# Kernel tuning notes

Hardware: AMD Instinct MI355X
Metric: run time of the kernel (lower is better)

The kernel has to match this reference:

```python
import jax, jax.numpy as jnp
import numpy as np

B, N, DIM = 4, 2048, 128
HEADS, HEAD = 8, 128
INNER = HEADS * HEAD  # 1024
EPS = 1e-5


def setup_inputs() -> dict:
    key = jax.random.key(0)
    k0, k1, k2 = jax.random.split(key, 3)
    return {
        "x": jax.random.normal(k0, (B, N, DIM), jnp.float32),
        "ln_gamma": jnp.ones((DIM,), jnp.float32),
        "ln_beta": jnp.zeros((DIM,), jnp.float32),
        "w_qkv": jax.random.normal(k1, (3 * INNER, DIM), jnp.float32) * (DIM ** -0.5),
        "w_out": jax.random.normal(k2, (DIM, INNER), jnp.float32) * (INNER ** -0.5),
        "b_out": jnp.zeros((DIM,), jnp.float32),
    }


def _rope(t):
    """lucidrains-style rotary embedding over full last dim of t: [b,h,n,d]."""
    n, d = t.shape[-2], t.shape[-1]
    inv_freq = 1.0 / (10000.0 ** (jnp.arange(0, d, 2, dtype=jnp.float32) / d))
    freqs = jnp.arange(n, dtype=jnp.float32)[:, None] * inv_freq[None, :]  # [n, d/2]
    freqs = jnp.repeat(freqs, 2, axis=-1)  # interleaved duplicate -> [n, d]
    cos, sin = jnp.cos(freqs), jnp.sin(freqs)
    # rotate_half on interleaved pairs: (x1, x2) -> (-x2, x1)
    x1, x2 = t[..., 0::2], t[..., 1::2]
    rot = jnp.stack((-x2, x1), axis=-1).reshape(t.shape)
    return t * cos + rot * sin


def reference(x, ln_gamma, ln_beta, w_qkv, w_out, b_out):
    # LayerNorm
    mu = x.mean(-1, keepdims=True)
    var = x.var(-1, keepdims=True)
    xn = (x - mu) * jax.lax.rsqrt(var + EPS) * ln_gamma + ln_beta
    # QKV projection (bias-free)
    qkv = jnp.einsum('bnd,ed->bne', xn, w_qkv)  # [B, N, 3*INNER]
    q, k, v = jnp.split(qkv, 3, axis=-1)
    to_heads = lambda t: t.reshape(B, N, HEADS, HEAD).transpose(0, 2, 1, 3)
    q, k, v = to_heads(q), to_heads(k), to_heads(v)  # [B, H, N, HEAD]
    # Partial RoPE: rotate all but the last token; last token stays unrotated
    q = jnp.concatenate([_rope(q[:, :, :-1]), q[:, :, -1:]], axis=2)
    k = jnp.concatenate([_rope(k[:, :, :-1]), k[:, :, -1:]], axis=2)
    scale = HEAD ** -0.5
    dots = jnp.einsum('bhid,bhjd->bhij', q, k) * scale  # [B, H, N, N]
    attn = jax.nn.softmax(dots, axis=-1)
    out = jnp.einsum('bhij,bhjd->bhid', attn, v)
    out = out.transpose(0, 2, 1, 3).reshape(B, N, INNER)
    return out @ w_out.T + b_out
```

## Files before the change

kernel.cpp:

```cpp
#include <hip/hip_runtime.h>
#include <hip/hip_bf16.h>
#include <hip/hip_fp16.h>

#define B_      4
#define N_      2048
#define DIM_    128
#define HEADS_  8
#define HEAD_   128
#define INNER_  1024
#define QKV_    3072
#define EPS_    1e-5f
#define SCALE_  0.08838834764831845f
#define ROPE_C  0.20762050593046015f

typedef __attribute__((ext_vector_type(8))) short short8;
typedef __attribute__((ext_vector_type(4))) short short4v;
typedef __attribute__((ext_vector_type(4))) float f32x4;


__device__ __forceinline__ unsigned short f2bf(float f) {
    unsigned u = __builtin_bit_cast(unsigned, f);
    u = (u + 0x7fffu + ((u >> 16) & 1u)) >> 16;
    return (unsigned short)u;
}
__device__ __forceinline__ float bf2f(unsigned short h) {
    unsigned u = ((unsigned)h) << 16;
    return __builtin_bit_cast(float, u);
}
__device__ __forceinline__ unsigned pk2(float a, float b) {
    return (unsigned)f2bf(a) | ((unsigned)f2bf(b) << 16);
}
__device__ __forceinline__ short4v pack4(const float* e) {
    __hip_bfloat162 h0 = __float22bfloat162_rn(make_float2(e[0], e[1]));
    __hip_bfloat162 h1 = __float22bfloat162_rn(make_float2(e[2], e[3]));
    uint2 u;
    __builtin_memcpy(&u.x, &h0, 4);
    __builtin_memcpy(&u.y, &h1, 4);
    return __builtin_bit_cast(short4v, u);
}

__global__ __launch_bounds__(256) void k_prep(
    const float* __restrict__ x, const float* __restrict__ g,
    const float* __restrict__ be, const float* __restrict__ w_qkv,
    const float* __restrict__ w_out, unsigned short* __restrict__ xnb,
    unsigned short* __restrict__ wqb, unsigned short* __restrict__ wob)
{
    const int bid = blockIdx.x;
    if (bid < 2048) {
        const int w = threadIdx.x >> 6, l = threadIdx.x & 63;
        const int row = bid * 4 + w;
        float2 v = *(const float2*)(x + (size_t)row * 128 + l * 2);
        float s = v.x + v.y, s2 = v.x * v.x + v.y * v.y;
#pragma unroll
        for (int off = 1; off < 64; off <<= 1) {
            s  += __shfl_xor(s, off);
            s2 += __shfl_xor(s2, off);
        }
        float mu = s * (1.f / 128.f);
        float var = s2 * (1.f / 128.f) - mu * mu;
        float rs = rsqrtf(var + EPS_);
        float2 gg = *(const float2*)(g + l * 2);
        float2 bb = *(const float2*)(be + l * 2);
        float ox = (v.x - mu) * rs * gg.x + bb.x;
        float oy = (v.y - mu) * rs * gg.y + bb.y;
        *(unsigned*)(xnb + (size_t)row * 128 + l * 2) = pk2(ox, oy);
    } else if (bid < 2240) {
        size_t i = ((size_t)(bid - 2048) * 256 + threadIdx.x) * 8;
        float4 f0 = *(const float4*)(w_qkv + i), f1 = *(const float4*)(w_qkv + i + 4);
        uint4 u = { pk2(f0.x, f0.y), pk2(f0.z, f0.w), pk2(f1.x, f1.y), pk2(f1.z, f1.w) };
        *(uint4*)(wqb + i) = u;
    } else {
        size_t i = ((size_t)(bid - 2240) * 256 + threadIdx.x) * 8;
        float4 f0 = *(const float4*)(w_out + i), f1 = *(const float4*)(w_out + i + 4);
        uint4 u = { pk2(f0.x, f0.y), pk2(f0.z, f0.w), pk2(f1.x, f1.y), pk2(f1.z, f1.w) };
        *(uint4*)(wob + i) = u;
    }
}

__global__ __launch_bounds__(256) void k_qkvf(
    const unsigned short* __restrict__ xnb, const unsigned short* __restrict__ wb,
    unsigned short* __restrict__ Q, unsigned short* __restrict__ K,
    unsigned short* __restrict__ Vt)
{
    __shared__ unsigned short lA[128 * 128];
    __shared__ unsigned short lB[128 * 128];
    const int t = threadIdx.x;
    const int wv = t >> 6, l = t & 63;
    const int lm = l & 15, quad = l >> 4;
    const int row0 = blockIdx.x * 128;
    const int by   = blockIdx.y;
    const int e0   = by * 128;

#pragma unroll
    for (int i = 0; i < 8; ++i) {
        int c = t + 256 * i;  int r = c >> 4, c8 = c & 15;
        int sc = (c8 ^ (r & 7)) * 8;
        *(uint4*)&lA[r * 128 + sc] =
            *(const uint4*)(xnb + (size_t)(row0 + r) * 128 + c8 * 8);
        *(uint4*)&lB[r * 128 + sc] =
            *(const uint4*)(wb + (size_t)(e0 + r) * 128 + c8 * 8);
    }
    __syncthreads();

    short8 af[2][4];
#pragma unroll
    for (int mt = 0; mt < 2; ++mt)
#pragma unroll
        for (int ks = 0; ks < 4; ++ks) {
            int r = wv * 32 + mt * 16 + lm;
            af[mt][ks] = *(short8*)&lA[r * 128 + (((ks * 4 + quad) ^ (r & 7)) << 3)];
        }

    f32x4 acc[2][8];
#pragma unroll
    for (int mt = 0; mt < 2; ++mt)
#pragma unroll
        for (int ct = 0; ct < 8; ++ct) acc[mt][ct] = (f32x4){0.f, 0.f, 0.f, 0.f};
#pragma unroll
    for (int ks = 0; ks < 4; ++ks) {
#pragma unroll
        for (int ct = 0; ct < 8; ++ct) {
            int r = ct * 16 + lm;
            short8 b = *(short8*)&lB[r * 128 + (((ks * 4 + quad) ^ (r & 7)) << 3)];
            acc[0][ct] = __builtin_amdgcn_mfma_f32_16x16x32_bf16(af[0][ks], b, acc[0][ct], 0, 0, 0);
            acc[1][ct] = __builtin_amdgcn_mfma_f32_16x16x32_bf16(af[1][ks], b, acc[1][ct], 0, 0, 0);
        }
    }
    __syncthreads();

    const int b  = row0 >> 11;
    const int n0 = row0 & (N_ - 1);
    const int h  = by & 7;
    const int bh = b * 8 + h;

    if (by < 16) {
#pragma unroll
        for (int mt = 0; mt < 2; ++mt)
#pragma unroll
            for (int ct = 0; ct < 8; ++ct)
#pragma unroll
                for (int r = 0; r < 4; ++r) {
                    int row = wv * 32 + mt * 16 + quad * 4 + r;
                    int chunk = ct * 2 + (lm >> 3);
                    lA[row * 128 + ((chunk ^ (row & 7)) << 3) + (lm & 7)] =
                        f2bf(acc[mt][ct][r]);
                }
        __syncthreads();

        const int r_loc = t >> 1, half = t & 1;
        const int n = n0 + r_loc;
        unsigned short* dst = (by < 8 ? Q : K) +
            ((size_t)bh * N_ + n) * HEAD_ + half * 64;
        const bool dorope = (n != N_ - 1);
#pragma unroll
        for (int j = 0; j < 8; ++j) {
            short8 vv = *(short8*)&lA[r_loc * 128 + (((half * 8 + j) ^ (r_loc & 7)) << 3)];
            if (dorope) {
                unsigned short* pv = (unsigned short*)&vv;
#pragma unroll
                for (int p = 0; p < 4; ++p) {
                    int i0 = half * 32 + j * 4 + p;
                    float invf = exp2f(-(float)i0 * ROPE_C);
                    float th = (float)n * invf;
                    float cs = __cosf(th), sn = __sinf(th);
                    float e = bf2f(pv[2 * p]), o = bf2f(pv[2 * p + 1]);
                    pv[2 * p]     = f2bf(e * cs - o * sn);
                    pv[2 * p + 1] = f2bf(o * cs + e * sn);
                }
            }
            *(short8*)(dst + j * 8) = vv;
        }
    } else {
#pragma unroll
        for (int mt = 0; mt < 2; ++mt)
#pragma unroll
            for (int ct = 0; ct < 8; ++ct)
#pragma unroll
                for (int r = 0; r < 4; ++r) {
                    int row = ct * 16 + lm;
                    int chunk = wv * 4 + quad;
                    lA[row * 128 + ((chunk ^ (row & 7)) << 3) + mt * 4 + r] =
                        f2bf(acc[mt][ct][r]);
                }
        __syncthreads();

        const int d = t >> 1, half = t & 1;
        unsigned short* dst = Vt + ((size_t)bh * HEAD_ + d) * N_ + n0 + half * 64;
#pragma unroll
        for (int j = 0; j < 8; ++j)
            *(short8*)(dst + j * 8) =
                *(short8*)&lA[d * 128 + (((half * 8 + j) ^ (d & 7)) << 3)];
    }
}

__global__ __launch_bounds__(256) void k_attn(
    const unsigned short* __restrict__ Q, const unsigned short* __restrict__ K,
    const unsigned short* __restrict__ Vt, unsigned short* __restrict__ Ob)
{
    __shared__ unsigned short lK[64 * 136];
    __shared__ unsigned short lV[128 * 68];

    const int t = threadIdx.x;
    const int w = t >> 6, l = t & 63;
    const int lm = l & 15, quad = l >> 4;
    const int bid = blockIdx.x;
    const int bh = bid & 31;
    const int qt = bid >> 5;
    const int n0 = qt * 128;
    const unsigned short* Qb = Q  + (size_t)bh * N_ * HEAD_;
    const unsigned short* Kb = K  + (size_t)bh * N_ * HEAD_;
    const unsigned short* Vb = Vt + (size_t)bh * N_ * HEAD_;

    short8 aq[2][4];
#pragma unroll
    for (int tt = 0; tt < 2; ++tt) {
        const unsigned short* qp =
            Qb + ((size_t)(n0 + tt * 64 + w * 16 + lm)) * 128 + quad * 8;
#pragma unroll
        for (int ks = 0; ks < 4; ++ks)
            aq[tt][ks] = *(const short8*)(qp + ks * 32);
    }

    f32x4 Oa[2][8];
#pragma unroll
    for (int tt = 0; tt < 2; ++tt)
#pragma unroll
        for (int i = 0; i < 8; ++i) Oa[tt][i] = (f32x4){0.f, 0.f, 0.f, 0.f};
    float ps0 = 0.f, ps1 = 0.f;
    const float C1 = SCALE_ * 1.44269504f;
    const float C0 = -23.08312f;

    short8 kr[4], vr[4];
#pragma unroll
    for (int i = 0; i < 4; ++i) {
        int c = t + 256 * i;
        kr[i] = *(const short8*)(Kb + ((size_t)(c >> 4)) * 128 + (c & 15) * 8);
        vr[i] = *(const short8*)(Vb + (size_t)(c >> 3) * N_ + (c & 7) * 8);
    }

    for (int jt = 0; jt < 32; ++jt) {
        __syncthreads();
#pragma unroll
        for (int i = 0; i < 4; ++i) {
            int c = t + 256 * i;
            *(short8*)&lK[(c >> 4) * 136 + (c & 15) * 8] = kr[i];
            *(short8*)&lV[(c >> 3) * 68  + (c & 7)  * 8] = vr[i];
        }
        __syncthreads();
        if (jt < 31) {
#pragma unroll
            for (int i = 0; i < 4; ++i) {
                int c = t + 256 * i;
                kr[i] = *(const short8*)(Kb + ((size_t)((jt + 1) * 64 + (c >> 4))) * 128 + (c & 15) * 8);
                vr[i] = *(const short8*)(Vb + (size_t)(c >> 3) * N_ + (jt + 1) * 64 + (c & 7) * 8);
            }
        }

        short4v pf0[4], pf1[4];
#pragma unroll
        for (int nb = 0; nb < 4; ++nb) {
            f32x4 st0 = (f32x4){0.f, 0.f, 0.f, 0.f};
            f32x4 st1 = (f32x4){0.f, 0.f, 0.f, 0.f};
#pragma unroll
            for (int ks = 0; ks < 4; ++ks) {
                short8 kf = *(short8*)&lK[(nb * 16 + lm) * 136 + ks * 32 + quad * 8];
                st0 = __builtin_amdgcn_mfma_f32_16x16x32_bf16(kf, aq[0][ks], st0, 0, 0, 0);
                st1 = __builtin_amdgcn_mfma_f32_16x16x32_bf16(kf, aq[1][ks], st1, 0, 0, 0);
            }
            float e0[4], e1[4];
#pragma unroll
            for (int r = 0; r < 4; ++r) {
                e0[r] = exp2f(st0[r] * C1 + C0);
                e1[r] = exp2f(st1[r] * C1 + C0);
                ps0 += e0[r];  ps1 += e1[r];
            }
            pf0[nb] = pack4(e0);
            pf1[nb] = pack4(e1);
        }

#pragma unroll
        for (int c2 = 0; c2 < 2; ++c2) {
            short8 ap0 = __builtin_shufflevector(pf0[2 * c2], pf0[2 * c2 + 1],
                                                 0, 1, 2, 3, 4, 5, 6, 7);
            short8 ap1 = __builtin_shufflevector(pf1[2 * c2], pf1[2 * c2 + 1],
                                                 0, 1, 2, 3, 4, 5, 6, 7);
#pragma unroll
            for (int nb8 = 0; nb8 < 8; ++nb8) {
                short8 bv = *(short8*)&lV[(nb8 * 16 + lm) * 68 + c2 * 32 + quad * 8];
                Oa[0][nb8] = __builtin_amdgcn_mfma_f32_16x16x32_bf16(ap0, bv, Oa[0][nb8], 0, 0, 0);
                Oa[1][nb8] = __builtin_amdgcn_mfma_f32_16x16x32_bf16(ap1, bv, Oa[1][nb8], 0, 0, 0);
            }
        }
    }

    ps0 += __shfl_xor(ps0, 16);  ps0 += __shfl_xor(ps0, 32);
    ps1 += __shfl_xor(ps1, 16);  ps1 += __shfl_xor(ps1, 32);

    const int b = bh >> 3, h = bh & 7;
#pragma unroll
    for (int tt = 0; tt < 2; ++tt)
#pragma unroll
        for (int r = 0; r < 4; ++r) {
            float lsum = __shfl(tt == 0 ? ps0 : ps1, (l & 48) | (quad * 4 + r));
            float il = 1.f / lsum;
            int n = n0 + tt * 64 + w * 16 + quad * 4 + r;
            unsigned short* op = Ob + ((size_t)b * N_ + n) * INNER_ + h * HEAD_ + lm;
#pragma unroll
            for (int nb8 = 0; nb8 < 8; ++nb8)
                op[nb8 * 16] = f2bf(Oa[tt][nb8][r] * il);
        }
}

__global__ __launch_bounds__(256) void k_proj(
    const unsigned short* __restrict__ Ob, const unsigned short* __restrict__ wob,
    const float* __restrict__ bias, float* __restrict__ out)
{
    __shared__ unsigned short lA[32 * 136];
    __shared__ unsigned short lB[64 * 136];
    float* lCf = (float*)lA;
    const int t = threadIdx.x;
    const int wv = t >> 6, l = t & 63;
    const int lm = l & 15, quad = l >> 4;
    const int rt = wv & 1, ch = wv >> 1;
    const int row0 = blockIdx.x * 32;
    const int e0   = blockIdx.y * 64;

    f32x4 acc[2];
#pragma unroll
    for (int ct = 0; ct < 2; ++ct) acc[ct] = (f32x4){0.f, 0.f, 0.f, 0.f};

    for (int kt = 0; kt < 8; ++kt) {
        __syncthreads();
#pragma unroll
        for (int i = 0; i < 2; ++i) {
            int c = t + 256 * i;  int r = c >> 4, c8 = c & 15;
            *(uint4*)&lA[r * 136 + c8 * 8] =
                *(const uint4*)(Ob + (size_t)(row0 + r) * 1024 + kt * 128 + c8 * 8);
        }
#pragma unroll
        for (int i = 0; i < 4; ++i) {
            int c = t + 256 * i;  int r = c >> 4, c8 = c & 15;
            *(uint4*)&lB[r * 136 + c8 * 8] =
                *(const uint4*)(wob + (size_t)(e0 + r) * 1024 + kt * 128 + c8 * 8);
        }
        __syncthreads();
        short8 a_[4];
#pragma unroll
        for (int ks = 0; ks < 4; ++ks)
            a_[ks] = *(short8*)&lA[(rt * 16 + lm) * 136 + ks * 32 + quad * 8];
#pragma unroll
        for (int ks = 0; ks < 4; ++ks)
#pragma unroll
            for (int ct = 0; ct < 2; ++ct) {
                short8 b = *(short8*)&lB[(ch * 32 + ct * 16 + lm) * 136 + ks * 32 + quad * 8];
                acc[ct] = __builtin_amdgcn_mfma_f32_16x16x32_bf16(a_[ks], b, acc[ct], 0, 0, 0);
            }
    }
    __syncthreads();
#pragma unroll
    for (int ct = 0; ct < 2; ++ct)
#pragma unroll
        for (int r = 0; r < 4; ++r)
            lCf[(rt * 16 + quad * 4 + r) * 68 + ch * 32 + ct * 16 + lm] = acc[ct][r];
    __syncthreads();
#pragma unroll
    for (int i = 0; i < 2; ++i) {
        int c = t + 256 * i;  int r = c >> 4, c4 = c & 15;
        float4 v = *(float4*)&lCf[r * 68 + c4 * 4];
        float4 b4 = *(const float4*)(bias + e0 + c4 * 4);
        v.x += b4.x; v.y += b4.y; v.z += b4.z; v.w += b4.w;
        *(float4*)(out + (size_t)(row0 + r) * 128 + e0 + c4 * 4) = v;
    }
}

extern "C" void kernel_launch(void* const* d_in, const int* in_sizes, int n_in,
                              void* d_out, int out_size, void* d_ws, size_t ws_size,
                              hipStream_t stream) {
    const float* x      = (const float*)d_in[0];
    const float* gamma  = (const float*)d_in[1];
    const float* beta   = (const float*)d_in[2];
    const float* w_qkv  = (const float*)d_in[3];
    const float* w_out  = (const float*)d_in[4];
    const float* b_out  = (const float*)d_in[5];
    float* out = (float*)d_out;
    char* wsb = (char*)d_ws;
    unsigned short* Q    = (unsigned short*)(wsb);
    unsigned short* K    = (unsigned short*)(wsb + (16ull << 20));
    unsigned short* Vt   = (unsigned short*)(wsb + (32ull << 20));
    unsigned short* Ob   = (unsigned short*)(wsb + (48ull << 20));
    unsigned short* xnb  = (unsigned short*)(wsb + (96ull << 20));
    unsigned short* wqb  = (unsigned short*)(wsb + (98ull << 20));
    unsigned short* wob  = (unsigned short*)(wsb + (99ull << 20));

    k_prep <<<dim3(2304),    256, 0, stream>>>(x, gamma, beta, w_qkv, w_out,
                                               xnb, wqb, wob);
    k_qkvf <<<dim3(64, 24),  256, 0, stream>>>(xnb, wqb, Q, K, Vt);
    k_attn <<<dim3(512),     256, 0, stream>>>(Q, K, Vt, Ob);
    k_proj <<<dim3(256, 2),  256, 0, stream>>>(Ob, wob, b_out, out);
}
```

Measured before the change: 188.7 us.

## Fuse LayerNorm and weight bf16 conversion into QKV and projection GEMM loads

Removes the separate prep kernel and instead computes LayerNorm on fp32 x while staging the A tile in the QKV GEMM, and converts fp32 weights to bf16 on the fly in both GEMMs. This saves one launch and the round trip of the bf16 intermediates through global memory. In exchange, each of the 24 column blocks redundantly recomputes LayerNorm for its rows, and the weight tiles are read as fp32, doubling the bytes loaded per tile. The epilogue staging moves from lA to lB so the A fragments are not overwritten.

```diff
diff --git a/kernel.cpp b/kernel.cpp
--- a/kernel.cpp
+++ b/kernel.cpp
@@ -39,46 +39,9 @@
     return __builtin_bit_cast(short4v, u);
 }
 
-__global__ __launch_bounds__(256) void k_prep(
+__global__ __launch_bounds__(256) void k_qkvf(
     const float* __restrict__ x, const float* __restrict__ g,
-    const float* __restrict__ be, const float* __restrict__ w_qkv,
-    const float* __restrict__ w_out, unsigned short* __restrict__ xnb,
-    unsigned short* __restrict__ wqb, unsigned short* __restrict__ wob)
-{
-    const int bid = blockIdx.x;
-    if (bid < 2048) {
-        const int w = threadIdx.x >> 6, l = threadIdx.x & 63;
-        const int row = bid * 4 + w;
-        float2 v = *(const float2*)(x + (size_t)row * 128 + l * 2);
-        float s = v.x + v.y, s2 = v.x * v.x + v.y * v.y;
-#pragma unroll
-        for (int off = 1; off < 64; off <<= 1) {
-            s  += __shfl_xor(s, off);
-            s2 += __shfl_xor(s2, off);
-        }
-        float mu = s * (1.f / 128.f);
-        float var = s2 * (1.f / 128.f) - mu * mu;
-        float rs = rsqrtf(var + EPS_);
-        float2 gg = *(const float2*)(g + l * 2);
-        float2 bb = *(const float2*)(be + l * 2);
-        float ox = (v.x - mu) * rs * gg.x + bb.x;
-        float oy = (v.y - mu) * rs * gg.y + bb.y;
-        *(unsigned*)(xnb + (size_t)row * 128 + l * 2) = pk2(ox, oy);
-    } else if (bid < 2240) {
-        size_t i = ((size_t)(bid - 2048) * 256 + threadIdx.x) * 8;
-        float4 f0 = *(const float4*)(w_qkv + i), f1 = *(const float4*)(w_qkv + i + 4);
-        uint4 u = { pk2(f0.x, f0.y), pk2(f0.z, f0.w), pk2(f1.x, f1.y), pk2(f1.z, f1.w) };
-        *(uint4*)(wqb + i) = u;
-    } else {
-        size_t i = ((size_t)(bid - 2240) * 256 + threadIdx.x) * 8;
-        float4 f0 = *(const float4*)(w_out + i), f1 = *(const float4*)(w_out + i + 4);
-        uint4 u = { pk2(f0.x, f0.y), pk2(f0.z, f0.w), pk2(f1.x, f1.y), pk2(f1.z, f1.w) };
-        *(uint4*)(wob + i) = u;
-    }
-}
-
-__global__ __launch_bounds__(256) void k_qkvf(
-    const unsigned short* __restrict__ xnb, const unsigned short* __restrict__ wb,
+    const float* __restrict__ be, const float* __restrict__ wq,
     unsigned short* __restrict__ Q, unsigned short* __restrict__ K,
     unsigned short* __restrict__ Vt)
 {
@@ -91,14 +54,63 @@
     const int by   = blockIdx.y;
     const int e0   = by * 128;
 
-#pragma unroll
-    for (int i = 0; i < 8; ++i) {
-        int c = t + 256 * i;  int r = c >> 4, c8 = c & 15;
-        int sc = (c8 ^ (r & 7)) * 8;
-        *(uint4*)&lA[r * 128 + sc] =
-            *(const uint4*)(xnb + (size_t)(row0 + r) * 128 + c8 * 8);
-        *(uint4*)&lB[r * 128 + sc] =
-            *(const uint4*)(wb + (size_t)(e0 + r) * 128 + c8 * 8);
+    {
+        const int r = t >> 1, half = t & 1;
+        const float* xr = x + (size_t)(row0 + r) * 128 + half * 64;
+        float sa[32], sq[32];
+#pragma unroll
+        for (int i = 0; i < 16; ++i) {
+            float4 v = *(const float4*)(xr + i * 4);
+            sa[2 * i]     = v.x + v.y;
+            sa[2 * i + 1] = v.z + v.w;
+            sq[2 * i]     = v.x * v.x + v.y * v.y;
+            sq[2 * i + 1] = v.z * v.z + v.w * v.w;
+        }
+#pragma unroll
+        for (int nlev = 16; nlev >= 1; nlev >>= 1)
+#pragma unroll
+            for (int j = 0; j < nlev; ++j) {
+                sa[j] = sa[2 * j] + sa[2 * j + 1];
+                sq[j] = sq[2 * j] + sq[2 * j + 1];
+            }
+        float s  = sa[0] + __shfl_xor(sa[0], 1);
+        float s2 = sq[0] + __shfl_xor(sq[0], 1);
+        float mu  = s * (1.f / 128.f);
+        float var = s2 * (1.f / 128.f) - mu * mu;
+        float rs  = rsqrtf(var + EPS_);
+#pragma unroll
+        for (int j = 0; j < 8; ++j) {
+            float4 a0 = *(const float4*)(xr + j * 8);
+            float4 a1 = *(const float4*)(xr + j * 8 + 4);
+            float4 g0 = *(const float4*)(g  + half * 64 + j * 8);
+            float4 g1 = *(const float4*)(g  + half * 64 + j * 8 + 4);
+            float4 b0 = *(const float4*)(be + half * 64 + j * 8);
+            float4 b1 = *(const float4*)(be + half * 64 + j * 8 + 4);
+            float e0_ = (a0.x - mu) * rs * g0.x + b0.x;
+            float e1_ = (a0.y - mu) * rs * g0.y + b0.y;
+            float e2_ = (a0.z - mu) * rs * g0.z + b0.z;
+            float e3_ = (a0.w - mu) * rs * g0.w + b0.w;
+            float e4_ = (a1.x - mu) * rs * g1.x + b1.x;
+            float e5_ = (a1.y - mu) * rs * g1.y + b1.y;
+            float e6_ = (a1.z - mu) * rs * g1.z + b1.z;
+            float e7_ = (a1.w - mu) * rs * g1.w + b1.w;
+            uint4 u = { pk2(e0_, e1_), pk2(e2_, e3_), pk2(e4_, e5_), pk2(e6_, e7_) };
+            int chunk = half * 8 + j;
+            *(uint4*)&lA[r * 128 + ((chunk ^ (r & 7)) << 3)] = u;
+        }
+    }
+    {
+        const int r = t >> 1, half = t & 1;
+        const float* wr = wq + (size_t)(e0 + r) * 128 + half * 64;
+#pragma unroll
+        for (int j = 0; j < 8; ++j) {
+            float4 a0 = *(const float4*)(wr + j * 8);
+            float4 a1 = *(const float4*)(wr + j * 8 + 4);
+            uint4 u = { pk2(a0.x, a0.y), pk2(a0.z, a0.w),
+                        pk2(a1.x, a1.y), pk2(a1.z, a1.w) };
+            int chunk = half * 8 + j;
+            *(uint4*)&lB[r * 128 + ((chunk ^ (r & 7)) << 3)] = u;
+        }
     }
     __syncthreads();
 
@@ -142,7 +154,7 @@
                 for (int r = 0; r < 4; ++r) {
                     int row = wv * 32 + mt * 16 + quad * 4 + r;
                     int chunk = ct * 2 + (lm >> 3);
-                    lA[row * 128 + ((chunk ^ (row & 7)) << 3) + (lm & 7)] =
+                    lB[row * 128 + ((chunk ^ (row & 7)) << 3) + (lm & 7)] =
                         f2bf(acc[mt][ct][r]);
                 }
         __syncthreads();
@@ -154,7 +166,7 @@
         const bool dorope = (n != N_ - 1);
 #pragma unroll
         for (int j = 0; j < 8; ++j) {
-            short8 vv = *(short8*)&lA[r_loc * 128 + (((half * 8 + j) ^ (r_loc & 7)) << 3)];
+            short8 vv = *(short8*)&lB[r_loc * 128 + (((half * 8 + j) ^ (r_loc & 7)) << 3)];
             if (dorope) {
                 unsigned short* pv = (unsigned short*)&vv;
 #pragma unroll
@@ -179,7 +191,7 @@
                 for (int r = 0; r < 4; ++r) {
                     int row = ct * 16 + lm;
                     int chunk = wv * 4 + quad;
-                    lA[row * 128 + ((chunk ^ (row & 7)) << 3) + mt * 4 + r] =
+                    lB[row * 128 + ((chunk ^ (row & 7)) << 3) + mt * 4 + r] =
                         f2bf(acc[mt][ct][r]);
                 }
         __syncthreads();
@@ -189,7 +201,7 @@
 #pragma unroll
         for (int j = 0; j < 8; ++j)
             *(short8*)(dst + j * 8) =
-                *(short8*)&lA[d * 128 + (((half * 8 + j) ^ (d & 7)) << 3)];
+                *(short8*)&lB[d * 128 + (((half * 8 + j) ^ (d & 7)) << 3)];
     }
 }
 
@@ -312,7 +324,7 @@
 }
 
 __global__ __launch_bounds__(256) void k_proj(
-    const unsigned short* __restrict__ Ob, const unsigned short* __restrict__ wob,
+    const unsigned short* __restrict__ Ob, const float* __restrict__ w_out,
     const float* __restrict__ bias, float* __restrict__ out)
 {
     __shared__ unsigned short lA[32 * 136];
@@ -337,11 +349,17 @@
             *(uint4*)&lA[r * 136 + c8 * 8] =
                 *(const uint4*)(Ob + (size_t)(row0 + r) * 1024 + kt * 128 + c8 * 8);
         }
-#pragma unroll
-        for (int i = 0; i < 4; ++i) {
-            int c = t + 256 * i;  int r = c >> 4, c8 = c & 15;
-            *(uint4*)&lB[r * 136 + c8 * 8] =
-                *(const uint4*)(wob + (size_t)(e0 + r) * 1024 + kt * 128 + c8 * 8);
+        {
+            const int r = t >> 2, q4 = t & 3;
+            const float* wr = w_out + (size_t)(e0 + r) * 1024 + kt * 128 + q4 * 32;
+#pragma unroll
+            for (int jj = 0; jj < 4; ++jj) {
+                float4 a0 = *(const float4*)(wr + jj * 8);
+                float4 a1 = *(const float4*)(wr + jj * 8 + 4);
+                uint4 u = { pk2(a0.x, a0.y), pk2(a0.z, a0.w),
+                            pk2(a1.x, a1.y), pk2(a1.z, a1.w) };
+                *(uint4*)&lB[r * 136 + q4 * 32 + jj * 8] = u;
+            }
         }
         __syncthreads();
         short8 a_[4];
@@ -388,13 +406,8 @@
     unsigned short* K    = (unsigned short*)(wsb + (16ull << 20));
     unsigned short* Vt   = (unsigned short*)(wsb + (32ull << 20));
     unsigned short* Ob   = (unsigned short*)(wsb + (48ull << 20));
-    unsigned short* xnb  = (unsigned short*)(wsb + (96ull << 20));
-    unsigned short* wqb  = (unsigned short*)(wsb + (98ull << 20));
-    unsigned short* wob  = (unsigned short*)(wsb + (99ull << 20));
-
-    k_prep <<<dim3(2304),    256, 0, stream>>>(x, gamma, beta, w_qkv, w_out,
-                                               xnb, wqb, wob);
-    k_qkvf <<<dim3(64, 24),  256, 0, stream>>>(xnb, wqb, Q, K, Vt);
-    k_attn <<<dim3(512),     256, 0, stream>>>(Q, K, Vt, Ob);
-    k_proj <<<dim3(256, 2),  256, 0, stream>>>(Ob, wob, b_out, out);
-}
+
+    k_qkvf <<<dim3(64, 24), 256, 0, stream>>>(x, gamma, beta, w_qkv, Q, K, Vt);
+    k_attn <<<dim3(512),    256, 0, stream>>>(Q, K, Vt, Ob);
+    k_proj <<<dim3(256, 2), 256, 0, stream>>>(Ob, w_out, b_out, out);
+}
```

Result: slower. 259.4 us (+37.5%).

## Switch attention kernel to 32x32x16 MFMA tiles with reshaped P/V fragments

Applied to the files above, without the earlier changes.

Rewrites the attention inner loop to use 32x32x16 bf16 MFMA instructions instead of 16x16x32. Each wave now owns 32 query rows, and scores, probabilities and output accumulators are laid out as 16-wide fragments. The V tile LDS stride moves from 68 to 72, and the V-transpose store in the QKV kernel is changed to match the new fragment layout. The goal is fewer MFMA issues and LDS fragment reads per unit of work, at the cost of different register pressure, a different LDS bank pattern, and scattered 2-byte output stores.

```diff
diff --git a/kernel.cpp b/kernel.cpp
--- a/kernel.cpp
+++ b/kernel.cpp
@@ -16,6 +16,7 @@
 typedef __attribute__((ext_vector_type(8))) short short8;
 typedef __attribute__((ext_vector_type(4))) short short4v;
 typedef __attribute__((ext_vector_type(4))) float f32x4;
+typedef __attribute__((ext_vector_type(16))) float f32x16;
 
 
 __device__ __forceinline__ unsigned short f2bf(float f) {
@@ -178,8 +179,9 @@
 #pragma unroll
                 for (int r = 0; r < 4; ++r) {
                     int row = ct * 16 + lm;
-                    int chunk = wv * 4 + quad;
-                    lA[row * 128 + ((chunk ^ (row & 7)) << 3) + mt * 4 + r] =
+                    int chunk = wv * 4 + mt * 2 + (quad & 1);
+                    int off   = (quad >> 1) * 4 + r;
+                    lA[row * 128 + ((chunk ^ (row & 7)) << 3) + off] =
                         f2bf(acc[mt][ct][r]);
                 }
         __syncthreads();
@@ -198,11 +200,11 @@
     const unsigned short* __restrict__ Vt, unsigned short* __restrict__ Ob)
 {
     __shared__ unsigned short lK[64 * 136];
-    __shared__ unsigned short lV[128 * 68];
+    __shared__ unsigned short lV[128 * 72];
 
     const int t = threadIdx.x;
     const int w = t >> 6, l = t & 63;
-    const int lm = l & 15, quad = l >> 4;
+    const int q32 = l & 31, hi = l >> 5;
     const int bid = blockIdx.x;
     const int bh = bid & 31;
     const int qt = bid >> 5;
@@ -211,22 +213,21 @@
     const unsigned short* Kb = K  + (size_t)bh * N_ * HEAD_;
     const unsigned short* Vb = Vt + (size_t)bh * N_ * HEAD_;
 
-    short8 aq[2][4];
-#pragma unroll
-    for (int tt = 0; tt < 2; ++tt) {
+    short8 aq[8];
+    {
         const unsigned short* qp =
-            Qb + ((size_t)(n0 + tt * 64 + w * 16 + lm)) * 128 + quad * 8;
-#pragma unroll
-        for (int ks = 0; ks < 4; ++ks)
-            aq[tt][ks] = *(const short8*)(qp + ks * 32);
-    }
-
-    f32x4 Oa[2][8];
-#pragma unroll
-    for (int tt = 0; tt < 2; ++tt)
-#pragma unroll
-        for (int i = 0; i < 8; ++i) Oa[tt][i] = (f32x4){0.f, 0.f, 0.f, 0.f};
-    float ps0 = 0.f, ps1 = 0.f;
+            Qb + (size_t)(n0 + w * 32 + q32) * 128 + hi * 8;
+#pragma unroll
+        for (int kc = 0; kc < 8; ++kc)
+            aq[kc] = *(const short8*)(qp + kc * 16);
+    }
+
+    f32x16 Oa[4];
+#pragma unroll
+    for (int i = 0; i < 4; ++i)
+        Oa[i] = (f32x16){0.f,0.f,0.f,0.f,0.f,0.f,0.f,0.f,
+                         0.f,0.f,0.f,0.f,0.f,0.f,0.f,0.f};
+    float ps = 0.f;
     const float C1 = SCALE_ * 1.44269504f;
     const float C0 = -23.08312f;
 
@@ -244,7 +245,7 @@
         for (int i = 0; i < 4; ++i) {
             int c = t + 256 * i;
             *(short8*)&lK[(c >> 4) * 136 + (c & 15) * 8] = kr[i];
-            *(short8*)&lV[(c >> 3) * 68  + (c & 7)  * 8] = vr[i];
+            *(short8*)&lV[(c >> 3) * 72  + (c & 7)  * 8] = vr[i];
         }
         __syncthreads();
         if (jt < 31) {
@@ -256,59 +257,69 @@
             }
         }
 
-        short4v pf0[4], pf1[4];
-#pragma unroll
-        for (int nb = 0; nb < 4; ++nb) {
-            f32x4 st0 = (f32x4){0.f, 0.f, 0.f, 0.f};
-            f32x4 st1 = (f32x4){0.f, 0.f, 0.f, 0.f};
-#pragma unroll
-            for (int ks = 0; ks < 4; ++ks) {
-                short8 kf = *(short8*)&lK[(nb * 16 + lm) * 136 + ks * 32 + quad * 8];
-                st0 = __builtin_amdgcn_mfma_f32_16x16x32_bf16(kf, aq[0][ks], st0, 0, 0, 0);
-                st1 = __builtin_amdgcn_mfma_f32_16x16x32_bf16(kf, aq[1][ks], st1, 0, 0, 0);
-            }
-            float e0[4], e1[4];
+        f32x16 st0 = (f32x16){0.f,0.f,0.f,0.f,0.f,0.f,0.f,0.f,
+                              0.f,0.f,0.f,0.f,0.f,0.f,0.f,0.f};
+        f32x16 st1 = st0;
+#pragma unroll
+        for (int kc = 0; kc < 8; ++kc) {
+            short8 kf0 = *(short8*)&lK[q32 * 136 + kc * 16 + hi * 8];
+            short8 kf1 = *(short8*)&lK[(32 + q32) * 136 + kc * 16 + hi * 8];
+            st0 = __builtin_amdgcn_mfma_f32_32x32x16_bf16(kf0, aq[kc], st0, 0, 0, 0);
+            st1 = __builtin_amdgcn_mfma_f32_32x32x16_bf16(kf1, aq[kc], st1, 0, 0, 0);
+        }
+
+        short8 pa[4];
+#pragma unroll
+        for (int T = 0; T < 2; ++T) {
+#pragma unroll
+            for (int g = 0; g < 2; ++g) {
+                float e[8];
+#pragma unroll
+                for (int j = 0; j < 8; ++j) {
+                    float s = T ? st1[8 * g + j] : st0[8 * g + j];
+                    e[j] = exp2f(s * C1 + C0);
+                    ps += e[j];
+                }
+                short4v lo = pack4(e);
+                short4v hh = pack4(e + 4);
+                pa[T * 2 + g] = __builtin_shufflevector(lo, hh, 0, 1, 2, 3, 4, 5, 6, 7);
+            }
+        }
+
+#pragma unroll
+        for (int dt = 0; dt < 4; ++dt) {
+            const int d = dt * 32 + q32;
+#pragma unroll
+            for (int kc = 0; kc < 4; ++kc) {
+                short8 bv = *(short8*)&lV[d * 72 + kc * 16 + hi * 8];
+                Oa[dt] = __builtin_amdgcn_mfma_f32_32x32x16_bf16(pa[kc], bv, Oa[dt], 0, 0, 0);
+            }
+        }
+    }
+
+    ps += __shfl_xor(ps, 32);
+    float inv = 1.f / ps;
+    float ilq[16];
+#pragma unroll
+    for (int m = 0; m < 4; ++m)
+#pragma unroll
+        for (int r = 0; r < 4; ++r)
+            ilq[m * 4 + r] = __shfl(inv, 4 * hi + r + 8 * m);
+
+    const int b = bh >> 3, h = bh & 7;
+#pragma unroll
+    for (int dt = 0; dt < 4; ++dt) {
+        const int d = dt * 32 + q32;
+#pragma unroll
+        for (int m = 0; m < 4; ++m)
 #pragma unroll
             for (int r = 0; r < 4; ++r) {
-                e0[r] = exp2f(st0[r] * C1 + C0);
-                e1[r] = exp2f(st1[r] * C1 + C0);
-                ps0 += e0[r];  ps1 += e1[r];
-            }
-            pf0[nb] = pack4(e0);
-            pf1[nb] = pack4(e1);
-        }
-
-#pragma unroll
-        for (int c2 = 0; c2 < 2; ++c2) {
-            short8 ap0 = __builtin_shufflevector(pf0[2 * c2], pf0[2 * c2 + 1],
-                                                 0, 1, 2, 3, 4, 5, 6, 7);
-            short8 ap1 = __builtin_shufflevector(pf1[2 * c2], pf1[2 * c2 + 1],
-                                                 0, 1, 2, 3, 4, 5, 6, 7);
-#pragma unroll
-            for (int nb8 = 0; nb8 < 8; ++nb8) {
-                short8 bv = *(short8*)&lV[(nb8 * 16 + lm) * 68 + c2 * 32 + quad * 8];
-                Oa[0][nb8] = __builtin_amdgcn_mfma_f32_16x16x32_bf16(ap0, bv, Oa[0][nb8], 0, 0, 0);
-                Oa[1][nb8] = __builtin_amdgcn_mfma_f32_16x16x32_bf16(ap1, bv, Oa[1][nb8], 0, 0, 0);
-            }
-        }
-    }
-
-    ps0 += __shfl_xor(ps0, 16);  ps0 += __shfl_xor(ps0, 32);
-    ps1 += __shfl_xor(ps1, 16);  ps1 += __shfl_xor(ps1, 32);
-
-    const int b = bh >> 3, h = bh & 7;
-#pragma unroll
-    for (int tt = 0; tt < 2; ++tt)
-#pragma unroll
-        for (int r = 0; r < 4; ++r) {
-            float lsum = __shfl(tt == 0 ? ps0 : ps1, (l & 48) | (quad * 4 + r));
-            float il = 1.f / lsum;
-            int n = n0 + tt * 64 + w * 16 + quad * 4 + r;
-            unsigned short* op = Ob + ((size_t)b * N_ + n) * INNER_ + h * HEAD_ + lm;
-#pragma unroll
-            for (int nb8 = 0; nb8 < 8; ++nb8)
-                op[nb8 * 16] = f2bf(Oa[tt][nb8][r] * il);
-        }
+                int q = 4 * hi + r + 8 * m;
+                int n = n0 + w * 32 + q;
+                Ob[((size_t)b * N_ + n) * INNER_ + h * HEAD_ + d] =
+                    f2bf(Oa[dt][m * 4 + r] * ilq[m * 4 + r]);
+            }
+    }
 }
 
 __global__ __launch_bounds__(256) void k_proj(
```

After: 191.2 us. About the same (+1.3%).
